# Kernel tuning notes

Hardware: AMD Instinct MI355X
Metric: run time of the kernel (lower is better)

The kernel has to match this reference:

```python
import jax, jax.numpy as jnp
import numpy as np

NEG_INF = -9.0e15

def setup_inputs() -> dict:
    key = jax.random.key(0)
    k1, k2, k3, k4, k5 = jax.random.split(key, 5)
    B, N, I, H, D = 4, 2048, 256, 4, 64  # batch, nodes, input_dim, heads, head_dim
    E = H * D
    X = jax.random.normal(k1, (B, N, I), dtype=jnp.float32)
    A = jax.random.randint(k2, (B, N, N), 0, 2, dtype=jnp.int32)
    # xavier_uniform with gain 1.38675
    g = 1.38675
    lim_W = g * np.sqrt(6.0 / (I + D))
    W = jax.random.uniform(k3, (H, I, D), minval=-lim_W, maxval=lim_W, dtype=jnp.float32)
    lim_a = g * np.sqrt(6.0 / (2 * D + 1))
    a = jax.random.uniform(k4, (H, 2 * D, 1), minval=-lim_a, maxval=lim_a, dtype=jnp.float32)
    lim_o = np.sqrt(1.0 / E)
    W_out = jax.random.uniform(k5, (E, E), minval=-lim_o, maxval=lim_o, dtype=jnp.float32)
    b_out = jnp.zeros((E,), dtype=jnp.float32)
    return {"X": X, "A": A, "W": W, "a": a, "W_out": W_out, "b_out": b_out}

def reference(X, A, W, a, W_out, b_out):
    B, N, _ = X.shape
    H_heads, _, D = W.shape
    # per-head projection: [b, h, n, d]
    Hp = jnp.einsum('bni,hid->bhnd', X, W)
    # additive attention scores (src/dst halves of a)
    H1 = jnp.einsum('bhnd,hd->bhn', Hp, a[:, :D, 0])   # [b,h,n]
    H2 = jnp.einsum('bhnd,hd->bhn', Hp, a[:, D:, 0])   # [b,h,n]
    E = jax.nn.leaky_relu(H1[:, :, :, None] + H2[:, :, None, :], negative_slope=0.2)  # [b,h,N,N]
    att = jnp.where(A[:, None, :, :] > 0, E, NEG_INF)
    # NOTE: faithful to original torch code: softmax over dim=1 (heads axis)
    att = jax.nn.softmax(att, axis=1)
    Hprime = jnp.einsum('bhNn,bhnd->bhNd', att, Hp)  # [b,h,N,d]
    # faithful raw reshape (no transpose), matching torch .reshape semantics
    Hprime = Hprime.reshape(B, N, H_heads * D)
    out = Hprime @ W_out.T + b_out
    return out
```

## Files before the change

### kernel.cpp

```cpp
#include <hip/hip_runtime.h>

constexpr int B = 4, N = 2048, I = 256, H = 4, D = 64, E = 256;
constexpr float LOG2E = 1.44269504088896340736f;

typedef __bf16 bf16x8 __attribute__((ext_vector_type(8)));
typedef float f32x4 __attribute__((ext_vector_type(4)));
typedef unsigned short us8 __attribute__((ext_vector_type(8)));

#if __has_builtin(__builtin_amdgcn_exp2f)
#define EXP2(x) __builtin_amdgcn_exp2f(x)
#else
#define EXP2(x) __expf((x) * 0.69314718055994530942f)
#endif

__device__ __forceinline__ unsigned short f2bf(float f) {
    unsigned u = __builtin_bit_cast(unsigned, f);
    u = (u + 0x7FFFu + ((u >> 16) & 1u)) >> 16;
    return (unsigned short)u;
}
__device__ __forceinline__ float bf2f(unsigned short s) {
    return __builtin_bit_cast(float, (unsigned)s << 16);
}

constexpr int CH = 4096;
constexpr int PROJ_BLKS = 256;
constexpr int PACK_BLKS = B * N / 4;

__global__ __launch_bounds__(256) void k_wconv(const float* __restrict__ Wo,
                                               const float* __restrict__ W,
                                               unsigned short* __restrict__ WoF,
                                               unsigned short* __restrict__ WfF) {
    int bid = blockIdx.x;
    int t = threadIdx.x;
    if (bid < 32) {
        int gid = bid * 256 + t;
        int l = gid & 63, ks = (gid >> 6) & 7, et = gid >> 9;
        int row = et * 16 + (l & 15);
        int col = ks * 32 + (l >> 4) * 8;
        const float* src = Wo + (size_t)row * E + col;
        us8 hi, lo;
        #pragma unroll
        for (int e = 0; e < 8; ++e) {
            float v = src[e];
            unsigned short hb = f2bf(v);
            hi[e] = hb;
            lo[e] = f2bf(v - bf2f(hb));
        }
        ((us8*)WoF)[gid] = hi;
        ((us8*)WoF)[8192 + gid] = lo;
    } else {
        int gid = (bid - 32) * 256 + t;
        int l = gid & 63, ks = (gid >> 6) & 7, et = gid >> 9;
        int c = et * 16 + (l & 15);
        int h = c >> 6, d = c & 63;
        int k0 = ks * 32 + (l >> 4) * 8;
        const float* src = W + ((size_t)h * I + k0) * D + d;
        us8 hi, lo;
        #pragma unroll
        for (int e = 0; e < 8; ++e) {
            float v = src[(size_t)e * D];
            unsigned short hb = f2bf(v);
            hi[e] = hb;
            lo[e] = f2bf(v - bf2f(hb));
        }
        ((us8*)WfF)[gid] = hi;
        ((us8*)WfF)[8192 + gid] = lo;
    }
}

__global__ __launch_bounds__(256) void k_prep(const float* __restrict__ X,
                                              const int* __restrict__ A,
                                              const float* __restrict__ a,
                                              const unsigned short* __restrict__ WfF,
                                              unsigned short* __restrict__ HpF,
                                              float* __restrict__ H1,
                                              float* __restrict__ H2i,
                                              unsigned int* __restrict__ Abits) {
    __shared__ float ldsT[4][16 * 132];

    int bid = blockIdx.x;
    int t = threadIdx.x;

    if (bid < PROJ_BLKS) {
        int wv = t >> 6, l = t & 63;
        int u = bid * 4 + wv;
        int eh = u & 1;
        int rt = u >> 1;
        int b = rt >> 7;
        int n0 = (rt & 127) * 16;
        int m = l & 15;
        int kh = l >> 4;

        const float* Xrow = X + ((size_t)b * N + n0 + m) * I + kh * 8;
        const us8* wf = (const us8*)WfF;

        f32x4 acc[8] = {};

        #pragma unroll
        for (int ks = 0; ks < 8; ++ks) {
            float4 xa = *(const float4*)(Xrow + ks * 32);
            float4 xb = *(const float4*)(Xrow + ks * 32 + 4);
            float xv[8] = {xa.x, xa.y, xa.z, xa.w, xb.x, xb.y, xb.z, xb.w};
            bf16x8 xh, xl;
            #pragma unroll
            for (int e = 0; e < 8; ++e) {
                unsigned short hb = f2bf(xv[e]);
                xh[e] = __builtin_bit_cast(__bf16, hb);
                xl[e] = __builtin_bit_cast(__bf16, f2bf(xv[e] - bf2f(hb)));
            }
            #pragma unroll
            for (int etl = 0; etl < 8; ++etl) {
                int et = eh * 8 + etl;
                bf16x8 wh = __builtin_bit_cast(bf16x8, wf[(size_t)(et * 8 + ks) * 64 + l]);
                bf16x8 wl = __builtin_bit_cast(bf16x8, wf[8192 + (size_t)(et * 8 + ks) * 64 + l]);
                acc[etl] = __builtin_amdgcn_mfma_f32_16x16x32_bf16(xh, wh, acc[etl], 0, 0, 0);
                acc[etl] = __builtin_amdgcn_mfma_f32_16x16x32_bf16(xl, wh, acc[etl], 0, 0, 0);
                acc[etl] = __builtin_amdgcn_mfma_f32_16x16x32_bf16(xh, wl, acc[etl], 0, 0, 0);
            }
        }

        float a1v[8], a2v[8];
        #pragma unroll
        for (int etl = 0; etl < 8; ++etl) {
            int c = eh * 128 + etl * 16 + m;
            int h = c >> 6, d = c & 63;
            a1v[etl] = a[h * (2 * D) + d];
            a2v[etl] = a[h * (2 * D) + D + d];
        }
        #pragma unroll
        for (int hh = 0; hh < 2; ++hh) {
            #pragma unroll
            for (int r = 0; r < 4; ++r) {
                float s1 = 0.f, s2 = 0.f;
                #pragma unroll
                for (int q = 0; q < 4; ++q) {
                    s1 += acc[hh * 4 + q][r] * a1v[hh * 4 + q];
                    s2 += acc[hh * 4 + q][r] * a2v[hh * 4 + q];
                }
                #pragma unroll
                for (int off = 1; off < 16; off <<= 1) {
                    s1 += __shfl_xor(s1, off, 64);
                    s2 += __shfl_xor(s2, off, 64);
                }
                if (m == 0) {
                    int hg = eh * 2 + hh;
                    int row = kh * 4 + r;
                    H1[(size_t)(b * H + hg) * N + n0 + row] = s1 * LOG2E;
                    H2i[((size_t)b * N + n0 + row) * H + hg] = s2 * LOG2E;
                }
            }
        }

        float* lw = ldsT[wv];
        #pragma unroll
        for (int etl = 0; etl < 8; ++etl)
            #pragma unroll
            for (int r = 0; r < 4; ++r)
                lw[(kh * 4 + r) * 132 + etl * 16 + m] = acc[etl][r];

        #pragma unroll
        for (int cc = 0; cc < 4; ++cc) {
            int ci = cc * 64 + l;
            int c_local = ci >> 1, q = ci & 1;
            us8 o;
            #pragma unroll
            for (int e = 0; e < 8; ++e)
                o[e] = f2bf(lw[(q * 8 + e) * 132 + c_local]);
            int cg = eh * 128 + c_local;
            int h = cg >> 6, d = cg & 63;
            int nb = n0 + q * 8;
            int jblk = nb >> 5, g = (nb >> 3) & 3;
            ((us8*)HpF)[(((size_t)(b * H + h) * 64 + jblk) * 4 + (d >> 4)) * 64 + ((d & 15) + 16 * g)] = o;
        }

    } else {
        int blk = bid - PROJ_BLKS;
        int w = blk * 4 + (t >> 6);
        int l = t & 63;
        int b = w >> 11;
        int i = w & 2047;
        const int4* Arow = (const int4*)(A + (size_t)w * N);
        unsigned int* dstb = Abits + (size_t)b * 64 * 2048 + i;
        #pragma unroll
        for (int c = 0; c < 8; ++c) {
            int4 v = Arow[c * 64 + l];
            unsigned nib = ((unsigned)v.x | ((unsigned)v.y << 1) |
                            ((unsigned)v.z << 2) | ((unsigned)v.w << 3)) << ((l & 7) * 4);
            nib |= __shfl_xor((int)nib, 1, 64);
            nib |= __shfl_xor((int)nib, 2, 64);
            nib |= __shfl_xor((int)nib, 4, 64);
            if ((l & 7) == 0) dstb[(size_t)(c * 8 + (l >> 3)) * 2048] = nib;
        }
    }
}

constexpr int NSTEP = 8;

__global__ __launch_bounds__(512) void k_agg(const unsigned int* __restrict__ Abits,
                                             const float* __restrict__ H1,
                                             const float* __restrict__ H2i,
                                             const unsigned short* __restrict__ HpF,
                                             const unsigned short* __restrict__ WoF,
                                             const float* __restrict__ bo,
                                             float* __restrict__ out) {
    __shared__ unsigned short red[8][CH];

    int bid = blockIdx.x;
    int b  = bid & 3;
    int it = bid >> 2;
    int t = threadIdx.x;
    int wv = t >> 6, l = t & 63;
    int i0 = it * 16;
    int jb = wv * 256;
    int jt0 = wv * 8;
    int row = l & 15;
    int kg  = l >> 4;

    float h1v[H];
    #pragma unroll
    for (int h = 0; h < H; ++h) h1v[h] = H1[(size_t)(b * H + h) * N + i0 + row];

    f32x4 acc[H][4] = {};

    const unsigned int* Abp = Abits + (size_t)b * 64 * 2048 + i0 + row;
    const float4* H2r = (const float4*)(H2i + ((size_t)b * N + jb + kg * 8) * H);
    const us8* Hf = (const us8*)HpF + ((size_t)(b * H) * 64 + jt0) * 256 + l;

    unsigned int aw = Abp[(size_t)jt0 * 2048];

    #pragma unroll 2
    for (int s = 0; s < NSTEP; ++s) {
        int sn = (s + 1 < NSTEP) ? (s + 1) : s;
        unsigned int awn = Abp[(size_t)(jt0 + sn) * 2048];

        bf16x8 af[H];
        #pragma unroll
        for (int e = 0; e < 8; ++e) {
            bool on = (aw >> (kg * 8 + e)) & 1u;
            float4 h2 = H2r[s * 32 + e];
            float v0 = h1v[0] + h2.x;
            float v1 = h1v[1] + h2.y;
            float v2 = h1v[2] + h2.z;
            float v3 = h1v[3] + h2.w;
            float s0 = on ? fmaxf(v0, 0.2f * v0) : 0.f;
            float s1 = on ? fmaxf(v1, 0.2f * v1) : 0.f;
            float s2 = on ? fmaxf(v2, 0.2f * v2) : 0.f;
            float s3 = on ? fmaxf(v3, 0.2f * v3) : 0.f;
            float e0 = EXP2(s0);
            float e1 = EXP2(s1);
            float e2 = EXP2(s2);
            float e3 = EXP2(s3);
            float zi = __builtin_amdgcn_rcpf(e0 + e1 + e2 + e3);
            af[0][e] = (__bf16)(e0 * zi);
            af[1][e] = (__bf16)(e1 * zi);
            af[2][e] = (__bf16)(e2 * zi);
            af[3][e] = (__bf16)(e3 * zi);
        }

        __builtin_amdgcn_s_setprio(1);
        #pragma unroll
        for (int h = 0; h < H; ++h) {
            #pragma unroll
            for (int nt = 0; nt < 4; ++nt) {
                bf16x8 bfr = __builtin_bit_cast(bf16x8, Hf[(size_t)h * 64 * 256 + s * 256 + nt * 64]);
                acc[h][nt] = __builtin_amdgcn_mfma_f32_16x16x32_bf16(af[h], bfr, acc[h][nt], 0, 0, 0);
            }
        }
        __builtin_amdgcn_s_setprio(0);

        aw = awn;
    }

    #pragma unroll
    for (int h = 0; h < H; ++h)
        #pragma unroll
        for (int nt = 0; nt < 4; ++nt)
            #pragma unroll
            for (int r = 0; r < 4; ++r)
                red[wv][(((h * 4 + nt) * 4 + r)) * 64 + l] = f2bf(acc[h][nt][r]);
    __syncthreads();

    {
        int idx8 = t * 8;
        float s8[8] = {0.f, 0.f, 0.f, 0.f, 0.f, 0.f, 0.f, 0.f};
        #pragma unroll
        for (int slot = 0; slot < 8; ++slot) {
            us8 raw = *(const us8*)&red[slot][idx8];
            #pragma unroll
            for (int e = 0; e < 8; ++e) s8[e] += bf2f(raw[e]);
        }
        us8 o;
        #pragma unroll
        for (int e = 0; e < 8; ++e) o[e] = f2bf(s8[e]);
        *(us8*)&red[0][idx8] = o;
    }
    __syncthreads();

    const us8* wf = (const us8*)WoF;
    f32x4 acc2[2] = {};

    #pragma unroll
    for (int ks = 0; ks < 8; ++ks) {
        int kk = ks * 32 + (l >> 4) * 8;
        int c = kk >> 6, d0 = kk & 63;
        int nt2 = d0 >> 4, dl = d0 & 15;
        int h2 = (l & 15) >> 2, g = (l & 15) & 3;
        int ridx = (((h2 * 4 + nt2) * 4 + c) * 64 + g * 16 + dl);
        bf16x8 afr = *(const bf16x8*)&red[0][ridx];

        #pragma unroll
        for (int etl = 0; etl < 2; ++etl) {
            int et = wv * 2 + etl;
            bf16x8 bh = __builtin_bit_cast(bf16x8, wf[(size_t)(et * 8 + ks) * 64 + l]);
            bf16x8 bl = __builtin_bit_cast(bf16x8, wf[8192 + (size_t)(et * 8 + ks) * 64 + l]);
            acc2[etl] = __builtin_amdgcn_mfma_f32_16x16x32_bf16(afr, bh, acc2[etl], 0, 0, 0);
            acc2[etl] = __builtin_amdgcn_mfma_f32_16x16x32_bf16(afr, bl, acc2[etl], 0, 0, 0);
        }
    }

    #pragma unroll
    for (int etl = 0; etl < 2; ++etl) {
        int e = (wv * 2 + etl) * 16 + (l & 15);
        float bias = bo[e];
        #pragma unroll
        for (int rr = 0; rr < 4; ++rr) {
            int mprime = (l >> 4) * 4 + rr;
            int nprime = (mprime >> 2) * 512 + it * 4 + (mprime & 3);
            out[((size_t)b * N + nprime) * E + e] = acc2[etl][rr] + bias;
        }
    }
}

extern "C" void kernel_launch(void* const* d_in, const int* in_sizes, int n_in,
                              void* d_out, int out_size, void* d_ws, size_t ws_size,
                              hipStream_t stream) {
    const float* X  = (const float*)d_in[0];
    const int*   A  = (const int*)d_in[1];
    const float* W  = (const float*)d_in[2];
    const float* a  = (const float*)d_in[3];
    const float* Wo = (const float*)d_in[4];
    const float* bo = (const float*)d_in[5];
    float* out = (float*)d_out;

    unsigned short* wsu = (unsigned short*)d_ws;
    unsigned short* HpF = wsu;
    float* H1  = (float*)(HpF + (size_t)B * H * D * N);
    float* H2i = H1 + B * H * N;
    unsigned int* Abits = (unsigned int*)(H2i + (size_t)B * N * H);
    unsigned short* WoF = (unsigned short*)(Abits + (size_t)B * 64 * 2048);
    unsigned short* WfF = WoF + 2 * 8192 * 8;

    k_wconv<<<dim3(64), dim3(256), 0, stream>>>(Wo, W, WoF, WfF);
    k_prep<<<dim3(PROJ_BLKS + PACK_BLKS), dim3(256), 0, stream>>>(
        X, A, a, WfF, HpF, H1, H2i, Abits);
    k_agg<<<dim3(B * 128), dim3(512), 0, stream>>>(Abits, H1, H2i, HpF, WoF, bo, out);
}
```

Baseline: 91.50 us.

## Split aggregation across two blocks per row tile with atomic last-block reduction

The aggregation kernel now splits the neighbor (j) dimension across two 256-thread blocks instead of one 512-thread block, doubling the grid. Each block writes its bf16 partial sums to a workspace buffer and increments a per-tile atomic counter. The last-arriving block combines both partials and runs the output projection GEMM with four tiles per wave. This aims to improve occupancy and load balance, at the cost of extra global traffic, a memset launch, and an extra bf16 rounding step.

```diff
diff --git a/kernel.cpp b/kernel.cpp
--- a/kernel.cpp
+++ b/kernel.cpp
@@ -196,23 +196,27 @@
 
 constexpr int NSTEP = 8;
 
-__global__ __launch_bounds__(512) void k_agg(const unsigned int* __restrict__ Abits,
+__global__ __launch_bounds__(256) void k_agg(const unsigned int* __restrict__ Abits,
                                              const float* __restrict__ H1,
                                              const float* __restrict__ H2i,
                                              const unsigned short* __restrict__ HpF,
                                              const unsigned short* __restrict__ WoF,
                                              const float* __restrict__ bo,
+                                             unsigned short* __restrict__ part,
+                                             unsigned int* __restrict__ flags,
                                              float* __restrict__ out) {
-    __shared__ unsigned short red[8][CH];
+    __shared__ unsigned short red[4][CH];
+    __shared__ int ldflag;
 
     int bid = blockIdx.x;
     int b  = bid & 3;
-    int it = bid >> 2;
+    int jh = (bid >> 2) & 1;
+    int it = bid >> 3;
     int t = threadIdx.x;
     int wv = t >> 6, l = t & 63;
     int i0 = it * 16;
-    int jb = wv * 256;
-    int jt0 = wv * 8;
+    int jb = jh * 1024 + wv * 256;
+    int jt0 = jb >> 5;
     int row = l & 15;
     int kg  = l >> 4;
 
@@ -280,24 +284,41 @@
                 red[wv][(((h * 4 + nt) * 4 + r)) * 64 + l] = f2bf(acc[h][nt][r]);
     __syncthreads();
 
-    {
-        int idx8 = t * 8;
-        float s8[8] = {0.f, 0.f, 0.f, 0.f, 0.f, 0.f, 0.f, 0.f};
-        #pragma unroll
-        for (int slot = 0; slot < 8; ++slot) {
-            us8 raw = *(const us8*)&red[slot][idx8];
-            #pragma unroll
-            for (int e = 0; e < 8; ++e) s8[e] += bf2f(raw[e]);
-        }
+    unsigned short* chunk = part + ((size_t)(b * 128 + it) * 2 + jh) * CH;
+    #pragma unroll
+    for (int k = 0; k < CH / 256; ++k) {
+        int idx = t + 256 * k;
+        float s = bf2f(red[0][idx]) + bf2f(red[1][idx]) + bf2f(red[2][idx]) + bf2f(red[3][idx]);
+        chunk[idx] = f2bf(s);
+    }
+    __syncthreads();
+
+    if (t == 0) {
+        int old = (int)__hip_atomic_fetch_add(&flags[b * 128 + it], 1u,
+                                              __ATOMIC_ACQ_REL, __HIP_MEMORY_SCOPE_AGENT);
+        ldflag = old;
+    }
+    __syncthreads();
+    if (ldflag == 0) return;
+    __threadfence();
+
+    unsigned short* afb = &red[0][0];
+    const us8* cc0 = (const us8*)(part + (size_t)(b * 128 + it) * 2 * CH);
+    const us8* cc1 = cc0 + CH / 8;
+    #pragma unroll
+    for (int kk = 0; kk < 2; ++kk) {
+        int idx = t + 256 * kk;
+        us8 p0 = cc0[idx];
+        us8 p1 = cc1[idx];
         us8 o;
         #pragma unroll
-        for (int e = 0; e < 8; ++e) o[e] = f2bf(s8[e]);
-        *(us8*)&red[0][idx8] = o;
+        for (int e = 0; e < 8; ++e) o[e] = f2bf(bf2f(p0[e]) + bf2f(p1[e]));
+        ((us8*)afb)[idx] = o;
     }
     __syncthreads();
 
     const us8* wf = (const us8*)WoF;
-    f32x4 acc2[2] = {};
+    f32x4 acc2[4] = {};
 
     #pragma unroll
     for (int ks = 0; ks < 8; ++ks) {
@@ -306,11 +327,11 @@
         int nt2 = d0 >> 4, dl = d0 & 15;
         int h2 = (l & 15) >> 2, g = (l & 15) & 3;
         int ridx = (((h2 * 4 + nt2) * 4 + c) * 64 + g * 16 + dl);
-        bf16x8 afr = *(const bf16x8*)&red[0][ridx];
-
-        #pragma unroll
-        for (int etl = 0; etl < 2; ++etl) {
-            int et = wv * 2 + etl;
+        bf16x8 afr = *(const bf16x8*)&afb[ridx];
+
+        #pragma unroll
+        for (int etl = 0; etl < 4; ++etl) {
+            int et = wv * 4 + etl;
             bf16x8 bh = __builtin_bit_cast(bf16x8, wf[(size_t)(et * 8 + ks) * 64 + l]);
             bf16x8 bl = __builtin_bit_cast(bf16x8, wf[8192 + (size_t)(et * 8 + ks) * 64 + l]);
             acc2[etl] = __builtin_amdgcn_mfma_f32_16x16x32_bf16(afr, bh, acc2[etl], 0, 0, 0);
@@ -319,8 +340,8 @@
     }
 
     #pragma unroll
-    for (int etl = 0; etl < 2; ++etl) {
-        int e = (wv * 2 + etl) * 16 + (l & 15);
+    for (int etl = 0; etl < 4; ++etl) {
+        int e = (wv * 4 + etl) * 16 + (l & 15);
         float bias = bo[e];
         #pragma unroll
         for (int rr = 0; rr < 4; ++rr) {
@@ -349,9 +370,13 @@
     unsigned int* Abits = (unsigned int*)(H2i + (size_t)B * N * H);
     unsigned short* WoF = (unsigned short*)(Abits + (size_t)B * 64 * 2048);
     unsigned short* WfF = WoF + 2 * 8192 * 8;
-
+    unsigned short* part = WfF + 2 * 8192 * 8;
+    unsigned int* flags = (unsigned int*)(part + (size_t)2 * 512 * CH);
+
+    hipMemsetAsync(flags, 0, 512 * sizeof(unsigned int), stream);
     k_wconv<<<dim3(64), dim3(256), 0, stream>>>(Wo, W, WoF, WfF);
     k_prep<<<dim3(PROJ_BLKS + PACK_BLKS), dim3(256), 0, stream>>>(
         X, A, a, WfF, HpF, H1, H2i, Abits);
-    k_agg<<<dim3(B * 128), dim3(512), 0, stream>>>(Abits, H1, H2i, HpF, WoF, bo, out);
-}
+    k_agg<<<dim3(2 * B * 128), dim3(256), 0, stream>>>(
+        Abits, H1, H2i, HpF, WoF, bo, part, flags, out);
+}
```

Result: slower. 189.4 us (+107.0%).
